# Kernel optimization log

Hardware: AMD Instinct MI355X
Metric: run time of the kernel (lower is better)

## Reference

```python
import jax, jax.numpy as jnp
import numpy as np

B, T, C, H = 2, 2048, 1024, 16  # batch, seq (== block_size), n_embd, n_head
HD = C // H  # head dim


def setup_inputs() -> dict:
    key = jax.random.key(0)
    k1, k2, k3 = jax.random.split(key, 3)
    x = jax.random.normal(k1, (B, T, C), dtype=jnp.float32)
    w_attn = jax.random.normal(k2, (C, 3 * C), dtype=jnp.float32) * (1.0 / np.sqrt(C))
    b_attn = jnp.zeros((3 * C,), dtype=jnp.float32)
    w_proj = jax.random.normal(k3, (C, C), dtype=jnp.float32) * (1.0 / np.sqrt(C))
    b_proj = jnp.zeros((C,), dtype=jnp.float32)
    return {"x": x, "w_attn": w_attn, "b_attn": b_attn, "w_proj": w_proj, "b_proj": b_proj}


def reference(x, w_attn, b_attn, w_proj, b_proj):
    # qkv projection: [B,T,3C]
    qkv = x @ w_attn + b_attn
    q, k, v = jnp.split(qkv, 3, axis=-1)
    # -> [B,H,T,HD]
    def to_heads(t):
        return t.reshape(B, T, H, HD).transpose(0, 2, 1, 3)
    q, k, v = to_heads(q), to_heads(k), to_heads(v)
    scale = 1.0 / np.sqrt(HD).astype(np.float32)
    # att: [B,H,T,T]
    att = jnp.einsum("bhqd,bhkd->bhqk", q, k) * scale
    causal = jnp.tril(jnp.ones((T, T), dtype=bool))
    att = jnp.where(causal[None, None], att, -jnp.inf)
    att = jax.nn.softmax(att, axis=-1)
    # y: [B,H,T,HD] -> [B,T,C]
    y = jnp.einsum("bhqk,bhkd->bhqd", att, v)
    y = y.transpose(0, 2, 1, 3).reshape(B, T, C)
    return y @ w_proj + b_proj
```

## Files before the change

kernel.cpp:

```cpp
#include <hip/hip_runtime.h>
#include <stdint.h>

#define Bb 2
#define Tt 2048
#define Cc 1024
#define Hh 16
#define HD 64
#define C3 3072

typedef __bf16 bf16x8 __attribute__((ext_vector_type(8)));
typedef float  f32x4  __attribute__((ext_vector_type(4)));
typedef unsigned short u16;
typedef u16 u16x8 __attribute__((ext_vector_type(8)));
typedef u16 u16x4 __attribute__((ext_vector_type(4)));

#define SCALE2 0.18033688f

__device__ __forceinline__ u16 f2bf(float f) {
  union { float f; unsigned u; } v; v.f = f;
  return (u16)((v.u + 0x7fffu + ((v.u >> 16) & 1u)) >> 16);
}
__device__ __forceinline__ u16 f2bf_fast(float f) {
  union { float f; unsigned u; } v; v.f = f;
  return (u16)((v.u + 0x8000u) >> 16);
}
__device__ __forceinline__ float bf2f(u16 a) {
  union { unsigned u; float f; } v; v.u = ((unsigned)a) << 16; return v.f;
}

__device__ __forceinline__ void gl2lds16(const void* g, void* s) {
  __builtin_amdgcn_global_load_lds(
      (__attribute__((address_space(1))) void*)(g),
      (__attribute__((address_space(3))) void*)(s), 16, 0, 0);
}

__device__ __forceinline__ bf16x8 ldb8(const u16* p) {
  return __builtin_bit_cast(bf16x8, *(const u16x8*)p);
}

__global__ __launch_bounds__(256)
void prep_kernel(const float* __restrict__ x, const float* __restrict__ w_attn,
                 const float* __restrict__ w_proj, u16* __restrict__ xb,
                 u16* __restrict__ wat, u16* __restrict__ wpt) {
  __shared__ u16 tile[64][65];
  const int blk = blockIdx.x;
  const int tid = threadIdx.x;
  if (blk < 4096) {
    int i = blk * 256 + tid;
    float4 v = ((const float4*)x)[i];
    u16x4 o = { f2bf(v.x), f2bf(v.y), f2bf(v.z), f2bf(v.w) };
    ((u16x4*)xb)[i] = o;
    return;
  }
  const float* in; u16* out; int R, C, c0, r0;
  if (blk < 4096 + 768) {
    int t = blk - 4096;
    in = w_attn; out = wat; R = 1024; C = 3072;
    c0 = (t % 48) * 64; r0 = (t / 48) * 64;
  } else {
    int t = blk - 4864;
    in = w_proj; out = wpt; R = 1024; C = 1024;
    c0 = (t & 15) * 64; r0 = (t >> 4) * 64;
  }
  int xx = tid & 63, yy = tid >> 6;
  #pragma unroll
  for (int rr = yy; rr < 64; rr += 4)
    tile[rr][xx] = f2bf(in[(size_t)(r0 + rr) * C + c0 + xx]);
  __syncthreads();
  #pragma unroll
  for (int rr = yy; rr < 64; rr += 4)
    out[(size_t)(c0 + rr) * R + r0 + xx] = tile[xx][rr];
}

template <int MODE, int BN>
__global__ __launch_bounds__(256)
void gemm_bt(const u16* __restrict__ A, const u16* __restrict__ Bt,
             const float* __restrict__ bias, void* __restrict__ Cout,
             u16* __restrict__ Vt, int M, int N, int K) {
  __shared__ u16 As[128 * 64];
  __shared__ u16 Bs[BN * 64];
  constexpr int JT = BN / 32;
  const int tid = threadIdx.x;
  const int ln  = tid & 63;
  const int w   = tid >> 6;
  const int wm  = w >> 1, wn = w & 1;
  const int l15 = ln & 15, lq = ln >> 4;
  const int swz = l15 & 7;
  const int m0 = blockIdx.y * 128, n0 = blockIdx.x * BN;

  f32x4 acc[4][JT];
  #pragma unroll
  for (int i = 0; i < 4; ++i)
    #pragma unroll
    for (int j = 0; j < JT; ++j)
      acc[i][j] = (f32x4){0.f, 0.f, 0.f, 0.f};

  for (int k0 = 0; k0 < K; k0 += 64) {
    #pragma unroll
    for (int i = 0; i < 4; ++i) {
      int s = i * 256 + tid;
      int row = s >> 3, cg = s & 7;
      gl2lds16(A + (size_t)(m0 + row) * K + k0 + ((cg ^ (row & 7)) * 8),
               (char*)As + (size_t)(i * 256 + w * 64) * 16);
    }
    #pragma unroll
    for (int i = 0; i < BN / 32; ++i) {
      int s = i * 256 + tid;
      int row = s >> 3, cg = s & 7;
      gl2lds16(Bt + (size_t)(n0 + row) * K + k0 + ((cg ^ (row & 7)) * 8),
               (char*)Bs + (size_t)(i * 256 + w * 64) * 16);
    }
    __syncthreads();
    #pragma unroll
    for (int ho = 0; ho < 2; ++ho) {
      bf16x8 af[4], bfr[JT];
      #pragma unroll
      for (int i = 0; i < 4; ++i)
        af[i] = ldb8(&As[(wm * 64 + i * 16 + l15) * 64 + ((ho * 4 + lq) ^ swz) * 8]);
      #pragma unroll
      for (int j = 0; j < JT; ++j)
        bfr[j] = ldb8(&Bs[(wn * (BN / 2) + j * 16 + l15) * 64 + ((ho * 4 + lq) ^ swz) * 8]);
      #pragma unroll
      for (int i = 0; i < 4; ++i)
        #pragma unroll
        for (int j = 0; j < JT; ++j)
          acc[i][j] = __builtin_amdgcn_mfma_f32_16x16x32_bf16(af[i], bfr[j], acc[i][j], 0, 0, 0);
    }
    __syncthreads();
  }

  if (MODE == 1 && n0 >= 2048) {
    #pragma unroll
    for (int i = 0; i < 4; ++i) {
      int rowb = m0 + wm * 64 + i * 16 + lq * 4;
      int b_ = rowb >> 11, t0 = rowb & 2047;
      int tl = t0 & 63;
      int c = tl >> 4, ll = (tl >> 2) & 3;
      int pos0 = (c >> 1) * 32 + ll * 8 + (c & 1) * 4;
      size_t tdst = (size_t)(t0 & ~63) + pos0;
      #pragma unroll
      for (int j = 0; j < JT; ++j) {
        int col = n0 + wn * (BN / 2) + j * 16 + l15;
        int hd = col - 2048;
        float bsv = bias[col];
        u16x4 pk;
        #pragma unroll
        for (int r = 0; r < 4; ++r) pk[r] = f2bf(acc[i][j][r] + bsv);
        *(u16x4*)&Vt[(size_t)(b_ * 1024 + hd) * Tt + tdst] = pk;
      }
    }
  } else {
    const int ldc = (MODE == 1) ? 2048 : N;
    #pragma unroll
    for (int i = 0; i < 4; ++i) {
      int row = m0 + wm * 64 + i * 16 + lq * 4;
      #pragma unroll
      for (int j = 0; j < JT; ++j) {
        int col = n0 + wn * (BN / 2) + j * 16 + l15;
        float bsv = bias[col];
        #pragma unroll
        for (int r = 0; r < 4; ++r) {
          float v = acc[i][j][r] + bsv;
          if (MODE == 1) ((u16*)Cout)[(size_t)(row + r) * ldc + col] = f2bf(v);
          else           ((float*)Cout)[(size_t)(row + r) * ldc + col] = v;
        }
      }
    }
  }
}


__device__ __forceinline__ bf16x8 packp(const f32x4& a, const f32x4& b) {
  u16x8 u = { f2bf_fast(a[0]), f2bf_fast(a[1]), f2bf_fast(a[2]), f2bf_fast(a[3]),
              f2bf_fast(b[0]), f2bf_fast(b[1]), f2bf_fast(b[2]), f2bf_fast(b[3]) };
  return __builtin_bit_cast(bf16x8, u);
}
__device__ __forceinline__ bf16x8 qscale(const u16* p) {
  u16x8 q = *(const u16x8*)p;
  u16x8 s;
  #pragma unroll
  for (int j = 0; j < 8; ++j) s[j] = f2bf(bf2f(q[j]) * SCALE2);
  return __builtin_bit_cast(bf16x8, s);
}

__global__ __launch_bounds__(256, 4)
void attn_fused(const u16* __restrict__ qk, const u16* __restrict__ vt,
                u16* __restrict__ y) {
  __shared__ u16 Ks[2][64 * 64];
  __shared__ u16 Vts[2][64 * 64];
  const int tid = threadIdx.x;
  const int ln = tid & 63, w = tid >> 6;
  const int l15 = ln & 15, lq = ln >> 4;
  const int swz = l15 & 7;
  const int bx = blockIdx.x;
  const int bh = bx & 31;
  const int h  = bh & 15, b = bh >> 4;
  const int rr_ = bx >> 8, g = (bx >> 5) & 7;
  const int qt = (rr_ == 0) ? 31 - g : (rr_ == 1) ? 16 + g : (rr_ == 2) ? 15 - g : g;
  const int q0 = qt * 64;
  const int q0w = q0 + w * 16;

  const u16* qbase = qk + (size_t)(b * Tt) * 2048 + h * HD;
  const u16* kbase = qk + (size_t)(b * Tt) * 2048 + 1024 + h * HD;
  const u16* vbase = vt + (size_t)(b * 1024 + h * HD) * Tt;

  const int s0 = tid, s1 = 256 + tid;
  const int koff0 = (s0 >> 3) * 2048 + (((s0 & 7) ^ ((s0 >> 3) & 7)) * 8);
  const int koff1 = (s1 >> 3) * 2048 + (((s1 & 7) ^ ((s1 >> 3) & 7)) * 8);

  const u16* qrA = qbase + (size_t)(q0w + l15) * 2048;
  bf16x8 qA0 = qscale(qrA + lq * 8), qA1 = qscale(qrA + 32 + lq * 8);

  f32x4 o[4];
  #pragma unroll
  for (int j = 0; j < 4; ++j) o[j] = (f32x4){0,0,0,0};
  float m = -__builtin_inff(), l = 0.f;
  const int qg = q0w + l15;

  const int nkv = qt + 1;

  {
    const u16* ksrc = kbase;
    const u16* vsrc = vbase;
    gl2lds16(ksrc + koff0, (char*)Ks[0] + w * 1024);
    gl2lds16(ksrc + koff1, (char*)Ks[0] + 4096 + w * 1024);
    gl2lds16(vsrc + koff0, (char*)Vts[0] + w * 1024);
    gl2lds16(vsrc + koff1, (char*)Vts[0] + 4096 + w * 1024);
  }

  for (int it = 0; it < nkv; ++it) {
    const int kk = it * 64;
    const int p = it & 1;
    __syncthreads();
    if (it + 1 < nkv) {
      const u16* ksrc = kbase + (size_t)(kk + 64) * 2048;
      const u16* vsrc = vbase + kk + 64;
      gl2lds16(ksrc + koff0, (char*)Ks[p ^ 1] + w * 1024);
      gl2lds16(ksrc + koff1, (char*)Ks[p ^ 1] + 4096 + w * 1024);
      gl2lds16(vsrc + koff0, (char*)Vts[p ^ 1] + w * 1024);
      gl2lds16(vsrc + koff1, (char*)Vts[p ^ 1] + 4096 + w * 1024);
    }
    const u16* KsB  = Ks[p];
    const u16* VtsB = Vts[p];

    f32x4 t[4];
    #pragma unroll
    for (int i = 0; i < 4; ++i) t[i] = (f32x4){0,0,0,0};
    #pragma unroll
    for (int i = 0; i < 4; ++i) {
      bf16x8 kf0 = ldb8(&KsB[(i * 16 + l15) * 64 + ((lq    ) ^ swz) * 8]);
      bf16x8 kf1 = ldb8(&KsB[(i * 16 + l15) * 64 + ((lq + 4) ^ swz) * 8]);
      t[i] = __builtin_amdgcn_mfma_f32_16x16x32_bf16(kf0, qA0, t[i], 0, 0, 0);
      t[i] = __builtin_amdgcn_mfma_f32_16x16x32_bf16(kf1, qA1, t[i], 0, 0, 0);
    }

    const bool lastI = (it == nkv - 1);
    if (lastI) {
      #pragma unroll
      for (int i = 0; i < 4; ++i)
        #pragma unroll
        for (int r = 0; r < 4; ++r) {
          int kv = kk + i * 16 + lq * 4 + r;
          if (kv > qg) t[i][r] = -__builtin_inff();
        }
    }
    float mx = t[0][0];
    #pragma unroll
    for (int i = 0; i < 4; ++i)
      #pragma unroll
      for (int r = 0; r < 4; ++r) mx = fmaxf(mx, t[i][r]);
    mx = fmaxf(mx, __shfl_xor(mx, 16));
    mx = fmaxf(mx, __shfl_xor(mx, 32));
    float mn = fmaxf(m, mx);
    float al = __builtin_amdgcn_exp2f(m - mn);
    float ps = 0.f;
    #pragma unroll
    for (int i = 0; i < 4; ++i)
      #pragma unroll
      for (int r = 0; r < 4; ++r) {
        float pp = __builtin_amdgcn_exp2f(t[i][r] - mn);
        t[i][r] = pp;
        ps += pp;
      }
    ps += __shfl_xor(ps, 16);
    ps += __shfl_xor(ps, 32);
    l = l * al + ps;
    m = mn;
    #pragma unroll
    for (int jd = 0; jd < 4; ++jd)
      #pragma unroll
      for (int r = 0; r < 4; ++r) o[jd][r] *= al;

    bf16x8 p0 = packp(t[0], t[1]), p1 = packp(t[2], t[3]);
    #pragma unroll
    for (int mf = 0; mf < 2; ++mf) {
      bf16x8 pb = mf ? p1 : p0;
      #pragma unroll
      for (int jd = 0; jd < 4; ++jd) {
        int d = jd * 16 + l15;
        bf16x8 vf = ldb8(&VtsB[d * 64 + ((mf * 4 + lq) ^ swz) * 8]);
        o[jd] = __builtin_amdgcn_mfma_f32_16x16x32_bf16(vf, pb, o[jd], 0, 0, 0);
      }
    }
  }

  float inv = 1.f / l;
  const size_t ybase = (size_t)(b * Tt + q0w + l15) * Cc + h * HD;
  #pragma unroll
  for (int jd = 0; jd < 4; ++jd) {
    u16x4 pk;
    #pragma unroll
    for (int r = 0; r < 4; ++r) pk[r] = f2bf(o[jd][r] * inv);
    *(u16x4*)&y[ybase + jd * 16 + lq * 4] = pk;
  }
}

extern "C" void kernel_launch(void* const* d_in, const int* in_sizes, int n_in,
                              void* d_out, int out_size, void* d_ws, size_t ws_size,
                              hipStream_t stream) {
  const float* x      = (const float*)d_in[0];
  const float* w_attn = (const float*)d_in[1];
  const float* b_attn = (const float*)d_in[2];
  const float* w_proj = (const float*)d_in[3];
  const float* b_proj = (const float*)d_in[4];
  float* out = (float*)d_out;

  char* ws = (char*)d_ws;
  u16* xb  = (u16*)(ws + 0);
  u16* wat = (u16*)(ws + 8388608);
  u16* wpt = (u16*)(ws + 14680064);
  u16* qkb = (u16*)(ws + 16777216);
  u16* vtb = (u16*)(ws + 33554432);
  u16* yb  = (u16*)(ws + 41943040);

  prep_kernel<<<5120, 256, 0, stream>>>(x, w_attn, w_proj, xb, wat, wpt);
  gemm_bt<1, 128><<<dim3(24, 32), 256, 0, stream>>>(xb, wat, b_attn, (void*)qkb, vtb, 4096, 3072, 1024);
  attn_fused<<<1024, 256, 0, stream>>>(qkb, vtb, yb);
  gemm_bt<0, 64><<<dim3(16, 32), 256, 0, stream>>>(yb, wpt, b_proj, (void*)out, nullptr, 4096, 1024, 1024);
}
```

Measured before the change: 186.2 us.

## Double-buffer GEMM LDS tiles with K-step 32 and precomputed load offsets

Restructures the bf16 GEMM main loop from a single-buffered 64-wide K tile with two barriers per step into a double-buffered 32-wide K tile. The next tile's global-to-LDS load is issued before the current tile's MFMAs, with one barrier per iteration. It also changes the swizzle to fit 32-element rows, precomputes global load offsets, and adds a launch-bounds occupancy hint of 4 blocks. The aim is to overlap global loads with compute, at the cost of twice as many loop iterations and barriers per unit of K and possible register pressure from the occupancy hint.

```diff
diff --git a/kernel.cpp b/kernel.cpp
--- a/kernel.cpp
+++ b/kernel.cpp
@@ -73,20 +73,34 @@
 }
 
 template <int MODE, int BN>
-__global__ __launch_bounds__(256)
+__global__ __launch_bounds__(256, 4)
 void gemm_bt(const u16* __restrict__ A, const u16* __restrict__ Bt,
              const float* __restrict__ bias, void* __restrict__ Cout,
              u16* __restrict__ Vt, int M, int N, int K) {
-  __shared__ u16 As[128 * 64];
-  __shared__ u16 Bs[BN * 64];
+  __shared__ u16 As[2][128 * 32];
+  __shared__ u16 Bs[2][BN * 32];
   constexpr int JT = BN / 32;
   const int tid = threadIdx.x;
   const int ln  = tid & 63;
   const int w   = tid >> 6;
   const int wm  = w >> 1, wn = w & 1;
   const int l15 = ln & 15, lq = ln >> 4;
-  const int swz = l15 & 7;
+  const int swz2 = (l15 >> 1) & 3;
   const int m0 = blockIdx.y * 128, n0 = blockIdx.x * BN;
+
+  int aoff[2], boff[BN / 128 + 1];
+  #pragma unroll
+  for (int i = 0; i < 2; ++i) {
+    int s = i * 256 + tid;
+    int row = s >> 2, cg = (s & 3) ^ ((s >> 3) & 3);
+    aoff[i] = (m0 + row) * K + cg * 8;
+  }
+  #pragma unroll
+  for (int i = 0; i < BN / 128 + 1; ++i) {
+    int s = i * 256 + tid;
+    int row = s >> 2, cg = (s & 3) ^ ((s >> 3) & 3);
+    boff[i] = (n0 + row) * K + cg * 8;
+  }
 
   f32x4 acc[4][JT];
   #pragma unroll
@@ -95,38 +109,40 @@
     for (int j = 0; j < JT; ++j)
       acc[i][j] = (f32x4){0.f, 0.f, 0.f, 0.f};
 
-  for (int k0 = 0; k0 < K; k0 += 64) {
-    #pragma unroll
-    for (int i = 0; i < 4; ++i) {
-      int s = i * 256 + tid;
-      int row = s >> 3, cg = s & 7;
-      gl2lds16(A + (size_t)(m0 + row) * K + k0 + ((cg ^ (row & 7)) * 8),
-               (char*)As + (size_t)(i * 256 + w * 64) * 16);
-    }
-    #pragma unroll
-    for (int i = 0; i < BN / 32; ++i) {
-      int s = i * 256 + tid;
-      int row = s >> 3, cg = s & 7;
-      gl2lds16(Bt + (size_t)(n0 + row) * K + k0 + ((cg ^ (row & 7)) * 8),
-               (char*)Bs + (size_t)(i * 256 + w * 64) * 16);
-    }
+  const int NK = K >> 5;
+  #pragma unroll
+  for (int i = 0; i < 2; ++i)
+    gl2lds16(A + aoff[i], (char*)As[0] + (size_t)(i * 256 + w * 64) * 16);
+  #pragma unroll
+  for (int i = 0; i < BN / 128 + 1; ++i)
+    gl2lds16(Bt + boff[i], (char*)Bs[0] + (size_t)(i * 256 + w * 64) * 16);
+
+  for (int it = 0; it < NK; ++it) {
+    const int p = it & 1;
     __syncthreads();
-    #pragma unroll
-    for (int ho = 0; ho < 2; ++ho) {
-      bf16x8 af[4], bfr[JT];
-      #pragma unroll
-      for (int i = 0; i < 4; ++i)
-        af[i] = ldb8(&As[(wm * 64 + i * 16 + l15) * 64 + ((ho * 4 + lq) ^ swz) * 8]);
+    if (it + 1 < NK) {
+      const int k0 = (it + 1) * 32;
+      #pragma unroll
+      for (int i = 0; i < 2; ++i)
+        gl2lds16(A + aoff[i] + k0, (char*)As[p ^ 1] + (size_t)(i * 256 + w * 64) * 16);
+      #pragma unroll
+      for (int i = 0; i < BN / 128 + 1; ++i)
+        gl2lds16(Bt + boff[i] + k0, (char*)Bs[p ^ 1] + (size_t)(i * 256 + w * 64) * 16);
+    }
+    const u16* AsB = As[p];
+    const u16* BsB = Bs[p];
+    bf16x8 af[4], bfr[JT];
+    #pragma unroll
+    for (int i = 0; i < 4; ++i)
+      af[i] = ldb8(&AsB[(wm * 64 + i * 16 + l15) * 32 + ((lq ^ swz2) * 8)]);
+    #pragma unroll
+    for (int j = 0; j < JT; ++j)
+      bfr[j] = ldb8(&BsB[(wn * (BN / 2) + j * 16 + l15) * 32 + ((lq ^ swz2) * 8)]);
+    #pragma unroll
+    for (int i = 0; i < 4; ++i)
       #pragma unroll
       for (int j = 0; j < JT; ++j)
-        bfr[j] = ldb8(&Bs[(wn * (BN / 2) + j * 16 + l15) * 64 + ((ho * 4 + lq) ^ swz) * 8]);
-      #pragma unroll
-      for (int i = 0; i < 4; ++i)
-        #pragma unroll
-        for (int j = 0; j < JT; ++j)
-          acc[i][j] = __builtin_amdgcn_mfma_f32_16x16x32_bf16(af[i], bfr[j], acc[i][j], 0, 0, 0);
-    }
-    __syncthreads();
+        acc[i][j] = __builtin_amdgcn_mfma_f32_16x16x32_bf16(af[i], bfr[j], acc[i][j], 0, 0, 0);
   }
 
   if (MODE == 1 && n0 >= 2048) {
@@ -220,12 +236,10 @@
   const int nkv = qt + 1;
 
   {
-    const u16* ksrc = kbase;
-    const u16* vsrc = vbase;
-    gl2lds16(ksrc + koff0, (char*)Ks[0] + w * 1024);
-    gl2lds16(ksrc + koff1, (char*)Ks[0] + 4096 + w * 1024);
-    gl2lds16(vsrc + koff0, (char*)Vts[0] + w * 1024);
-    gl2lds16(vsrc + koff1, (char*)Vts[0] + 4096 + w * 1024);
+    gl2lds16(kbase + koff0, (char*)Ks[0] + w * 1024);
+    gl2lds16(kbase + koff1, (char*)Ks[0] + 4096 + w * 1024);
+    gl2lds16(vbase + koff0, (char*)Vts[0] + w * 1024);
+    gl2lds16(vbase + koff1, (char*)Vts[0] + 4096 + w * 1024);
   }
 
   for (int it = 0; it < nkv; ++it) {
```

Measured after the change: 178.7 us. 4.1% less time.
